# Performance work log

Measured on AMD Instinct MI355X. Metric: run time of the kernel, lower is better.

The kernel has to match this reference:

```python
import jax, jax.numpy as jnp
import numpy as np

B, L, HID = 2, 2048, 2048
N_HEAD, HEAD_DIM, N_KV = 32, 64, 8
N_Q_PER_KV = N_HEAD // N_KV  # 4
SCALE = 0.125  # 1/sqrt(HEAD_DIM)
PAD_START = L - 256  # last 256 key positions are padding
NEG = -1e9


def setup_inputs() -> dict:
    key = jax.random.key(0)
    ks = jax.random.split(key, 8)
    query = jax.random.normal(ks[0], (B, L, HID), jnp.float32)
    kv = jax.random.normal(ks[1], (B, L, HID), jnp.float32)
    # additive causal mask (0 on/below diagonal, -1e9 above)
    i = jnp.arange(L)
    attn_mask = jnp.where(i[None, :] > i[:, None], NEG, 0.0).astype(jnp.float32)
    # key padding mask: True == padded position
    key_padding_mask = (i[None, :] >= PAD_START) & jnp.ones((B, 1), bool)
    s = 0.02
    Wq = jax.random.normal(ks[2], (HID, N_HEAD * HEAD_DIM), jnp.float32) * s
    bq = jnp.zeros((N_HEAD * HEAD_DIM,), jnp.float32)
    Wkv = jax.random.normal(ks[3], (HID, 2 * N_KV * HEAD_DIM), jnp.float32) * s
    bkv = jnp.zeros((2 * N_KV * HEAD_DIM,), jnp.float32)
    Wo = jax.random.normal(ks[4], (N_HEAD * HEAD_DIM, HID), jnp.float32) * s
    bo = jnp.zeros((HID,), jnp.float32)
    return {"query": query, "kv": kv, "Wq": Wq, "bq": bq, "Wkv": Wkv,
            "bkv": bkv, "Wo": Wo, "bo": bo, "attn_mask": attn_mask,
            "key_padding_mask": key_padding_mask}


def reference(query, kv, Wq, bq, Wkv, bkv, Wo, bo, attn_mask, key_padding_mask):
    b, l, _ = query.shape
    q = (query @ Wq + bq).reshape(b, l, N_HEAD, HEAD_DIM).transpose(0, 2, 1, 3)  # [B,H,L,D]
    kvp = kv @ Wkv + bkv                                   # [B,L,2*NKV*D]
    k, v = jnp.split(kvp, 2, axis=-1)
    k = k.reshape(b, l, N_KV, HEAD_DIM)
    v = v.reshape(b, l, N_KV, HEAD_DIM)
    # GQA: repeat_interleave KV heads to match Q heads
    k = jnp.repeat(k, N_Q_PER_KV, axis=2).transpose(0, 2, 1, 3)  # [B,H,L,D]
    v = jnp.repeat(v, N_Q_PER_KV, axis=2).transpose(0, 2, 1, 3)
    qk = jnp.einsum('bhqd,bhkd->bhqk', q, k) * SCALE
    qk = qk + attn_mask                                     # additive mask
    qk = jnp.where(key_padding_mask[:, None, None, :], NEG, qk)
    p = jax.nn.softmax(qk.astype(jnp.float32), axis=-1).astype(q.dtype)
    attn = jnp.einsum('bhqk,bhkd->bhqd', p, v)
    attn = attn.transpose(0, 2, 1, 3).reshape(b, l, N_HEAD * HEAD_DIM)
    out = attn @ Wo + bo
    return out
```

## Files before the change

kernel.cpp:

```cpp
#include <hip/hip_runtime.h>
#include <stdint.h>

#define L_SEQ 2048
#define HID 2048
#define PADK 1792
#define QSCALE 0.18033688011112042f

typedef unsigned short us_t;
typedef __attribute__((ext_vector_type(8))) short bf16x8;
typedef __attribute__((ext_vector_type(4))) float f32x4;

__device__ __forceinline__ float bf2f(us_t u) {
    union { unsigned int i; float f; } c; c.i = ((unsigned int)u) << 16; return c.f;
}
__device__ __forceinline__ us_t f2bf(float f) {
    union { float f; unsigned int i; } c; c.f = f;
    unsigned int i = c.i;
    return (us_t)((i + 0x7FFFu + ((i >> 16) & 1u)) >> 16);
}
__device__ __forceinline__ unsigned int pk_bf16(float a, float b) {
#if __has_builtin(__builtin_amdgcn_cvt_pk_bf16_f32)
    auto r = __builtin_amdgcn_cvt_pk_bf16_f32(a, b);
    unsigned int u; __builtin_memcpy(&u, &r, 4); return u;
#else
    return (unsigned int)f2bf(a) | ((unsigned int)f2bf(b) << 16);
#endif
}
__device__ __forceinline__ float fast_exp2(float x) {
#if __has_builtin(__builtin_amdgcn_exp2f)
    return __builtin_amdgcn_exp2f(x);
#else
    return exp2f(x);
#endif
}
__device__ __forceinline__ void gload_lds16(const us_t* g, us_t* l) {
    __builtin_amdgcn_global_load_lds((const __attribute__((address_space(1))) void*)g,
                                     (__attribute__((address_space(3))) void*)l, 16, 0, 0);
}
__device__ __forceinline__ int detect_bf16(const unsigned int* q) {
    __shared__ int sc[4];
    unsigned int v = q[threadIdx.x & 255];
    unsigned int e = (v >> 7) & 0xFFu;
    unsigned long long bb = __ballot(e >= 112u && e <= 133u);
    int cnt = __popcll(bb);
    if ((threadIdx.x & 63) == 0) sc[threadIdx.x >> 6] = cnt;
    __syncthreads();
    return (sc[0] + sc[1] + sc[2] + sc[3]) > 128;
}

__global__ __launch_bounds__(256) void prep(const unsigned int* __restrict__ qdet,
                                            const void* __restrict__ query,
                                            const void* __restrict__ kvsrc,
                                            const void* __restrict__ Wq,
                                            const void* __restrict__ Wkv,
                                            const void* __restrict__ Wo,
                                            us_t* __restrict__ Aq, us_t* __restrict__ Akv,
                                            us_t* __restrict__ Wqt, us_t* __restrict__ Wkvt,
                                            us_t* __restrict__ Wot) {
    __shared__ us_t tile[64][65];
    const int bf = detect_bf16(qdet);
    int id = blockIdx.x;
    if (id < 8192) {
        const void* s = (id < 4096) ? query : kvsrc;
        us_t* d       = (id < 4096) ? Aq : Akv;
        int cid = (id & 4095) * 256 + threadIdx.x;
        if (bf) {
            ((bf16x8*)d)[cid] = ((const bf16x8*)s)[cid];
        } else {
            const float* sp = (const float*)s + (size_t)cid * 8;
            f32x4 a = *(const f32x4*)sp, b2 = *(const f32x4*)(sp + 4);
            union { bf16x8 v; unsigned int dw[4]; } o;
            o.dw[0] = pk_bf16(a[0], a[1]);   o.dw[1] = pk_bf16(a[2], a[3]);
            o.dw[2] = pk_bf16(b2[0], b2[1]); o.dw[3] = pk_bf16(b2[2], b2[3]);
            ((bf16x8*)d)[cid] = o.v;
        }
        return;
    }
    id -= 8192;
    const void* s; us_t* d; int R, C, bx, by;
    if (id < 1024)      { s = Wq;  d = Wqt;  R = 2048; C = 2048; bx = id & 31; by = id >> 5; }
    else if (id < 1536) { id -= 1024; s = Wkv; d = Wkvt; R = 2048; C = 1024; bx = id & 15; by = id >> 4; }
    else                { id -= 1536; s = Wo;  d = Wot;  R = 2048; C = 2048; bx = id & 31; by = id >> 5; }
    const int c0 = bx * 64, r0 = by * 64;
    #pragma unroll
    for (int i = 0; i < 16; ++i) {
        int idx = threadIdx.x + i * 256;
        int r = idx >> 6, c = idx & 63;
        tile[r][c] = bf ? ((const us_t*)s)[(size_t)(r0 + r) * C + c0 + c]
                        : f2bf(((const float*)s)[(size_t)(r0 + r) * C + c0 + c]);
    }
    __syncthreads();
    #pragma unroll
    for (int i = 0; i < 16; ++i) {
        int idx = threadIdx.x + i * 256;
        int c = idx >> 6, r = idx & 63;
        d[(size_t)(c0 + c) * R + r0 + r] = tile[r][c];
    }
}

__device__ __forceinline__ void gemm_core(const us_t* __restrict__ A,
                                          const us_t* __restrict__ Bt,
                                          int K, int bm, int bn, int t,
                                          us_t (&As)[2][8192], us_t (&Bs)[2][8192],
                                          f32x4 (&acc)[4][4]) {
    const int w = t >> 6, lane = t & 63, l15 = lane & 15, quad = lane >> 4;
    const int wm = (w & 1) * 64, wn = (w >> 1) * 64;
    int rA[4], cA[4];
    #pragma unroll
    for (int i = 0; i < 4; ++i) {
        int p = (w * 4 + i) * 64 + lane;
        int row = p >> 3, cs = p & 7;
        rA[i] = row; cA[i] = (cs ^ (row & 7)) * 8;
    }
    #pragma unroll
    for (int i = 0; i < 4; ++i) {
        gload_lds16(A  + (size_t)(bm + rA[i]) * K + cA[i], &As[0][(w * 4 + i) * 512]);
        gload_lds16(Bt + (size_t)(bn + rA[i]) * K + cA[i], &Bs[0][(w * 4 + i) * 512]);
    }
    int pb = 0;
    for (int k0 = 0; k0 < K; k0 += 64) {
        __syncthreads();
        if (k0 + 64 < K) {
            #pragma unroll
            for (int i = 0; i < 4; ++i) {
                gload_lds16(A  + (size_t)(bm + rA[i]) * K + k0 + 64 + cA[i], &As[pb ^ 1][(w * 4 + i) * 512]);
                gload_lds16(Bt + (size_t)(bn + rA[i]) * K + k0 + 64 + cA[i], &Bs[pb ^ 1][(w * 4 + i) * 512]);
            }
        }
        #pragma unroll
        for (int ki = 0; ki < 2; ++ki) {
            bf16x8 af[4], bfr[4];
            #pragma unroll
            for (int mt = 0; mt < 4; ++mt) {
                int row = wm + mt * 16 + l15;
                int cs  = (ki * 4 + quad) ^ (row & 7);
                af[mt] = *(const bf16x8*)&As[pb][row * 64 + cs * 8];
            }
            #pragma unroll
            for (int nt = 0; nt < 4; ++nt) {
                int row = wn + nt * 16 + l15;
                int cs  = (ki * 4 + quad) ^ (row & 7);
                bfr[nt] = *(const bf16x8*)&Bs[pb][row * 64 + cs * 8];
            }
            #pragma unroll
            for (int mt = 0; mt < 4; ++mt)
                #pragma unroll
                for (int nt = 0; nt < 4; ++nt)
                    acc[mt][nt] = __builtin_amdgcn_mfma_f32_16x16x32_bf16(af[mt], bfr[nt], acc[mt][nt], 0, 0, 0);
        }
        pb ^= 1;
    }
}

__global__ __launch_bounds__(256, 2) void qkv_gemm(const unsigned int* __restrict__ qdet,
                                                   const us_t* __restrict__ Aq,
                                                   const us_t* __restrict__ Akv,
                                                   const us_t* __restrict__ Wqt,
                                                   const us_t* __restrict__ Wkvt,
                                                   const void* __restrict__ bq,
                                                   const void* __restrict__ bkv,
                                                   us_t* __restrict__ Qm,
                                                   us_t* __restrict__ Km,
                                                   us_t* __restrict__ Vg) {
    __shared__ us_t As[2][8192], Bs[2][8192];
    const int bf = detect_bf16(qdet);
    const int t = threadIdx.x;
    const int w = t >> 6, lane = t & 63, l15 = lane & 15, quad = lane >> 4;
    const int wm = (w & 1) * 64, wn = (w >> 1) * 64;
    f32x4 acc[4][4];
    #pragma unroll
    for (int i = 0; i < 4; ++i)
        #pragma unroll
        for (int j = 0; j < 4; ++j) acc[i][j] = (f32x4){0.f, 0.f, 0.f, 0.f};

    int id = blockIdx.x;
    if (id < 512) {
        const int bm = (id >> 4) * 128, bn = (id & 15) * 128;
        gemm_core(Aq, Wqt, 2048, bm, bn, t, As, Bs, acc);
        #pragma unroll
        for (int nt = 0; nt < 4; ++nt) {
            int col = bn + wn + nt * 16 + l15;
            float bvv = bf ? bf2f(((const us_t*)bq)[col]) : ((const float*)bq)[col];
            #pragma unroll
            for (int mt = 0; mt < 4; ++mt)
                #pragma unroll
                for (int r = 0; r < 4; ++r) {
                    int row = bm + wm + mt * 16 + quad * 4 + r;
                    Qm[(size_t)row * 2048 + col] = f2bf((acc[mt][nt][r] + bvv) * QSCALE);
                }
        }
    } else {
        id -= 512;
        const int bm = (id >> 3) * 128, bn = (id & 7) * 128;
        gemm_core(Akv, Wkvt, 2048, bm, bn, t, As, Bs, acc);
        if (bn < 512) {
            #pragma unroll
            for (int nt = 0; nt < 4; ++nt) {
                int col = bn + wn + nt * 16 + l15;
                float bvv = bf ? bf2f(((const us_t*)bkv)[col]) : ((const float*)bkv)[col];
                #pragma unroll
                for (int mt = 0; mt < 4; ++mt)
                    #pragma unroll
                    for (int r = 0; r < 4; ++r) {
                        int row = bm + wm + mt * 16 + quad * 4 + r;
                        Km[(size_t)row * 512 + col] = f2bf(acc[mt][nt][r] + bvv);
                    }
            }
        } else {
            us_t* ldsT = &As[0][0];
            const int b2 = bm >> 11, tok0 = bm & 2047;
            #pragma unroll
            for (int hh = 0; hh < 2; ++hh) {
                __syncthreads();
                if ((w >> 1) == hh) {
                    #pragma unroll
                    for (int nt = 0; nt < 4; ++nt) {
                        int col = bn + hh * 64 + nt * 16 + l15;
                        float bvv = bf ? bf2f(((const us_t*)bkv)[col]) : ((const float*)bkv)[col];
                        int c2 = nt * 16 + l15;
                        #pragma unroll
                        for (int mt = 0; mt < 4; ++mt)
                            #pragma unroll
                            for (int r = 0; r < 4; ++r) {
                                int tok = wm + mt * 16 + quad * 4 + r;
                                ldsT[c2 * 136 + tok] = f2bf(acc[mt][nt][r] + bvv);
                            }
                    }
                }
                __syncthreads();
                size_t vrow0 = (size_t)(b2 * 512 + (bn - 512) + hh * 64);
                #pragma unroll
                for (int j = 0; j < 4; ++j) {
                    int idx = t + j * 256;
                    int c2 = idx >> 4, ch = idx & 15;
                    bf16x8 vv = *(const bf16x8*)&ldsT[c2 * 136 + ch * 8];
                    *(bf16x8*)(Vg + (vrow0 + c2) * (size_t)2048 + tok0 + ch * 8) = vv;
                }
            }
        }
    }
}

__global__ __launch_bounds__(256, 2) void o_gemm(const unsigned int* __restrict__ qdet,
                                                 const us_t* __restrict__ Ao,
                                                 const us_t* __restrict__ Wot,
                                                 const void* __restrict__ bo,
                                                 void* __restrict__ Out) {
    __shared__ us_t As[2][8192], Bs[2][8192];
    const int bf = detect_bf16(qdet);
    const int t = threadIdx.x;
    const int w = t >> 6, lane = t & 63, l15 = lane & 15, quad = lane >> 4;
    const int wm = (w & 1) * 64, wn = (w >> 1) * 64;
    const int bm = blockIdx.y * 128, bn = blockIdx.x * 128;
    f32x4 acc[4][4];
    #pragma unroll
    for (int i = 0; i < 4; ++i)
        #pragma unroll
        for (int j = 0; j < 4; ++j) acc[i][j] = (f32x4){0.f, 0.f, 0.f, 0.f};
    gemm_core(Ao, Wot, 2048, bm, bn, t, As, Bs, acc);
    #pragma unroll
    for (int nt = 0; nt < 4; ++nt) {
        int col = bn + wn + nt * 16 + l15;
        float bvv = bf ? bf2f(((const us_t*)bo)[col]) : ((const float*)bo)[col];
        #pragma unroll
        for (int mt = 0; mt < 4; ++mt)
            #pragma unroll
            for (int r = 0; r < 4; ++r) {
                int row = bm + wm + mt * 16 + quad * 4 + r;
                float v = acc[mt][nt][r] + bvv;
                if (bf) ((us_t*)Out)[(size_t)row * 2048 + col] = f2bf(v);
                else    ((float*)Out)[(size_t)row * 2048 + col] = v;
            }
    }
}

__device__ __forceinline__ void qk_exp(const bf16x8 kb[2][4], const bf16x8 qf[2][2],
                                       int q0, int k0, int l15, int quad,
                                       bf16x8 pa[2][2]) {
    f32x4 sa[2][4];
    #pragma unroll
    for (int mt = 0; mt < 2; ++mt)
        #pragma unroll
        for (int nt = 0; nt < 4; ++nt) sa[mt][nt] = (f32x4){0.f, 0.f, 0.f, 0.f};
    #pragma unroll
    for (int ki = 0; ki < 2; ++ki)
        #pragma unroll
        for (int mt = 0; mt < 2; ++mt)
            #pragma unroll
            for (int nt = 0; nt < 4; ++nt)
                sa[mt][nt] = __builtin_amdgcn_mfma_f32_16x16x32_bf16(kb[ki][nt], qf[mt][ki], sa[mt][nt], 0, 0, 0);
    const bool nm = (k0 + 63 > q0);
    #pragma unroll
    for (int mt = 0; mt < 2; ++mt) {
        const int qrow = q0 + mt * 16 + l15;
        union { bf16x8 v; unsigned int dw[4]; } u;
        #pragma unroll
        for (int k2 = 0; k2 < 2; ++k2) {
            #pragma unroll
            for (int hf = 0; hf < 2; ++hf) {
                const int nt = k2 * 2 + hf;
                const int keyb = k0 + k2 * 32 + hf * 4 + quad * 8;
                float e[4];
                #pragma unroll
                for (int r = 0; r < 4; ++r) {
                    float s = sa[mt][nt][r];
                    if (nm && (keyb + r > qrow)) s = -1e30f;
                    e[r] = fast_exp2(s);
                }
                u.dw[hf * 2]     = pk_bf16(e[0], e[1]);
                u.dw[hf * 2 + 1] = pk_bf16(e[2], e[3]);
            }
            pa[mt][k2] = u.v;
        }
    }
}

__global__ __launch_bounds__(256, 2) void attn_mfma(const us_t* __restrict__ Q,
                                                    const us_t* __restrict__ Km,
                                                    const us_t* __restrict__ Vg,
                                                    us_t* __restrict__ Am) {
    __shared__ us_t Ks[2][4096];
    __shared__ us_t Vt[2][4096];

    const int bid = blockIdx.x;
    const int pr  = bid & 31;
    const int kvh = (bid >> 5) & 7;
    const int b   = bid >> 8;
    const int t = threadIdx.x, w = t >> 6, lane = t & 63, l15 = lane & 15, quad = lane >> 4;
    const int h = kvh * 4 + w;
    const int q0h = 2016 - 32 * pr, q0l = 32 * pr;
    const int kend0 = min(q0h + 32, PADK), kend1 = min(q0l + 32, PADK);

    bf16x8 ones;
    #pragma unroll
    for (int j = 0; j < 8; ++j) ones[j] = (short)0x3F80;

    const us_t* Kbase = Km + (size_t)(b * L_SEQ) * 512 + kvh * 64;
    const us_t* Vbase = Vg + (size_t)(b * 512 + kvh * 64) * L_SEQ;

    size_t ksrc[2], vsrc[2];
    #pragma unroll
    for (int i = 0; i < 2; ++i) {
        int idx = (w * 2 + i) * 64 + lane;
        int p = idx >> 3, cs = idx & 7, c = cs ^ (p & 7);
        int gk = (p & 0x23) | ((p & 0x0C) << 1) | ((p & 0x10) >> 2);
        ksrc[i] = (size_t)gk * 512 + c * 8;
        vsrc[i] = (size_t)p * 2048 + c * 8;
    }

    bf16x8 qfh[2][2], qfl[2][2];
    #pragma unroll
    for (int mt = 0; mt < 2; ++mt)
        #pragma unroll
        for (int ki = 0; ki < 2; ++ki) {
            qfh[mt][ki] = *(const bf16x8*)(Q + (size_t)(b * L_SEQ + q0h + mt * 16 + l15) * HID
                                             + h * 64 + ki * 32 + quad * 8);
            qfl[mt][ki] = *(const bf16x8*)(Q + (size_t)(b * L_SEQ + q0l + mt * 16 + l15) * HID
                                             + h * 64 + ki * 32 + quad * 8);
        }

    f32x4 oah[2][4], oal[2][4], lah[2], lal[2];
    #pragma unroll
    for (int mt = 0; mt < 2; ++mt) {
        lah[mt] = (f32x4){0.f, 0.f, 0.f, 0.f};
        lal[mt] = (f32x4){0.f, 0.f, 0.f, 0.f};
        #pragma unroll
        for (int dn = 0; dn < 4; ++dn) {
            oah[mt][dn] = (f32x4){0.f, 0.f, 0.f, 0.f};
            oal[mt][dn] = (f32x4){0.f, 0.f, 0.f, 0.f};
        }
    }

    #pragma unroll
    for (int i = 0; i < 2; ++i) {
        gload_lds16(Kbase + ksrc[i], &Ks[0][(w * 2 + i) * 512]);
        gload_lds16(Vbase + vsrc[i], &Vt[0][(w * 2 + i) * 512]);
    }

    int pb = 0;
    for (int k0 = 0; k0 < kend0; k0 += 64) {
        __syncthreads();
        if (k0 + 64 < kend0) {
            #pragma unroll
            for (int i = 0; i < 2; ++i) {
                gload_lds16(Kbase + (size_t)(k0 + 64) * 512 + ksrc[i], &Ks[pb ^ 1][(w * 2 + i) * 512]);
                gload_lds16(Vbase + (k0 + 64) + vsrc[i],               &Vt[pb ^ 1][(w * 2 + i) * 512]);
            }
        }
        const bool dolight = (k0 < kend1);

        bf16x8 kb[2][4];
        #pragma unroll
        for (int ki = 0; ki < 2; ++ki)
            #pragma unroll
            for (int nt = 0; nt < 4; ++nt) {
                int row = nt * 16 + l15;
                int cs  = (ki * 4 + quad) ^ (row & 7);
                kb[ki][nt] = *(const bf16x8*)&Ks[pb][row * 64 + cs * 8];
            }

        bf16x8 pah[2][2], pal[2][2];
        qk_exp(kb, qfh, q0h, k0, l15, quad, pah);
        if (dolight) qk_exp(kb, qfl, q0l, k0, l15, quad, pal);

        bf16x8 vb[2][4];
        #pragma unroll
        for (int k2 = 0; k2 < 2; ++k2)
            #pragma unroll
            for (int dn = 0; dn < 4; ++dn) {
                int d  = dn * 16 + l15;
                int cs = (k2 * 4 + quad) ^ (d & 7);
                vb[k2][dn] = *(const bf16x8*)&Vt[pb][d * 64 + cs * 8];
            }

        #pragma unroll
        for (int k2 = 0; k2 < 2; ++k2)
            #pragma unroll
            for (int mt = 0; mt < 2; ++mt) {
                lah[mt] = __builtin_amdgcn_mfma_f32_16x16x32_bf16(pah[mt][k2], ones, lah[mt], 0, 0, 0);
                #pragma unroll
                for (int dn = 0; dn < 4; ++dn)
                    oah[mt][dn] = __builtin_amdgcn_mfma_f32_16x16x32_bf16(pah[mt][k2], vb[k2][dn], oah[mt][dn], 0, 0, 0);
            }
        if (dolight) {
            #pragma unroll
            for (int k2 = 0; k2 < 2; ++k2)
                #pragma unroll
                for (int mt = 0; mt < 2; ++mt) {
                    lal[mt] = __builtin_amdgcn_mfma_f32_16x16x32_bf16(pal[mt][k2], ones, lal[mt], 0, 0, 0);
                    #pragma unroll
                    for (int dn = 0; dn < 4; ++dn)
                        oal[mt][dn] = __builtin_amdgcn_mfma_f32_16x16x32_bf16(pal[mt][k2], vb[k2][dn], oal[mt][dn], 0, 0, 0);
                }
        }
        pb ^= 1;
    }

    #pragma unroll
    for (int mt = 0; mt < 2; ++mt)
        #pragma unroll
        for (int r = 0; r < 4; ++r) {
            float invh = 1.0f / lah[mt][r];
            float invl = 1.0f / lal[mt][r];
            int rowh = q0h + mt * 16 + quad * 4 + r;
            int rowl = q0l + mt * 16 + quad * 4 + r;
            #pragma unroll
            for (int dn = 0; dn < 4; ++dn) {
                Am[(size_t)(b * L_SEQ + rowh) * HID + h * 64 + dn * 16 + l15] =
                    f2bf(oah[mt][dn][r] * invh);
                Am[(size_t)(b * L_SEQ + rowl) * HID + h * 64 + dn * 16 + l15] =
                    f2bf(oal[mt][dn][r] * invl);
            }
        }
}

extern "C" void kernel_launch(void* const* d_in, const int* in_sizes, int n_in,
                              void* d_out, int out_size, void* d_ws, size_t ws_size,
                              hipStream_t stream) {
    const void* query = d_in[0];
    const void* kv    = d_in[1];
    const void* Wq    = d_in[2];
    const void* bq    = d_in[3];
    const void* Wkv   = d_in[4];
    const void* bkv   = d_in[5];
    const void* Wo    = d_in[6];
    const void* bo    = d_in[7];
    const unsigned int* qdet = (const unsigned int*)query;

    char* p = (char*)d_ws;
    us_t* Qm   = (us_t*)p;                p += (size_t)4096 * 2048 * 2;
    us_t* Km   = (us_t*)p;                p += (size_t)4096 * 512 * 2;
    us_t* Vg   = (us_t*)p;                p += (size_t)1024 * 2048 * 2;
    us_t* AqAm = (us_t*)p;                p += (size_t)4096 * 2048 * 2;
    us_t* Akv  = (us_t*)p;                p += (size_t)4096 * 2048 * 2;
    us_t* Wqt  = (us_t*)p;                p += (size_t)2048 * 2048 * 2;
    us_t* Wkvt = (us_t*)p;                p += (size_t)1024 * 2048 * 2;
    us_t* Wot  = (us_t*)p;

    dim3 blk(256);
    prep<<<dim3(10752), blk, 0, stream>>>(qdet, query, kv, Wq, Wkv, Wo,
                                          AqAm, Akv, Wqt, Wkvt, Wot);
    qkv_gemm<<<dim3(768), blk, 0, stream>>>(qdet, AqAm, Akv, Wqt, Wkvt, bq, bkv,
                                            Qm, Km, Vg);
    attn_mfma<<<dim3(512), blk, 0, stream>>>(Qm, Km, Vg, AqAm);
    o_gemm<<<dim3(16, 32), blk, 0, stream>>>(qdet, AqAm, Wot, bo, d_out);
}
```

Baseline: 361.0 us.

## Rewrite QKV GEMM as 256x256 tile, 8-wave kernel with phased prefetch

Replaces the 128x128, 4-wave QKV projection GEMM with a 256x256-tile, 512-thread kernel. The K loop is split into eight phases per pair of k-tiles, each interleaving partial global-to-LDS staging with MFMA bursts, using raw barriers, explicit vmcnt waits and setprio. The aim is more reuse per loaded tile and better overlap of loads with compute. The trade-off is 128KB of LDS, which may limit occupancy to one block per CU, and only 192 blocks on a 256-CU device.

```diff
diff --git a/kernel.cpp b/kernel.cpp
--- a/kernel.cpp
+++ b/kernel.cpp
@@ -46,6 +46,19 @@
     if ((threadIdx.x & 63) == 0) sc[threadIdx.x >> 6] = cnt;
     __syncthreads();
     return (sc[0] + sc[1] + sc[2] + sc[3]) > 128;
+}
+__device__ __forceinline__ int detect_bf16_512(const unsigned int* q) {
+    __shared__ int sc[8];
+    unsigned int v = q[threadIdx.x & 255];
+    unsigned int e = (v >> 7) & 0xFFu;
+    unsigned long long bb = __ballot(e >= 112u && e <= 133u);
+    int cnt = __popcll(bb);
+    if ((threadIdx.x & 63) == 0) sc[threadIdx.x >> 6] = cnt;
+    __syncthreads();
+    int s = 0;
+    #pragma unroll
+    for (int i = 0; i < 8; ++i) s += sc[i];
+    return s > 256;
 }
 
 __global__ __launch_bounds__(256) void prep(const unsigned int* __restrict__ qdet,
@@ -98,61 +111,42 @@
     }
 }
 
-__device__ __forceinline__ void gemm_core(const us_t* __restrict__ A,
-                                          const us_t* __restrict__ Bt,
-                                          int K, int bm, int bn, int t,
-                                          us_t (&As)[2][8192], us_t (&Bs)[2][8192],
-                                          f32x4 (&acc)[4][4]) {
-    const int w = t >> 6, lane = t & 63, l15 = lane & 15, quad = lane >> 4;
-    const int wm = (w & 1) * 64, wn = (w >> 1) * 64;
-    int rA[4], cA[4];
-    #pragma unroll
-    for (int i = 0; i < 4; ++i) {
-        int p = (w * 4 + i) * 64 + lane;
-        int row = p >> 3, cs = p & 7;
-        rA[i] = row; cA[i] = (cs ^ (row & 7)) * 8;
-    }
-    #pragma unroll
-    for (int i = 0; i < 4; ++i) {
-        gload_lds16(A  + (size_t)(bm + rA[i]) * K + cA[i], &As[0][(w * 4 + i) * 512]);
-        gload_lds16(Bt + (size_t)(bn + rA[i]) * K + cA[i], &Bs[0][(w * 4 + i) * 512]);
-    }
-    int pb = 0;
-    for (int k0 = 0; k0 < K; k0 += 64) {
-        __syncthreads();
-        if (k0 + 64 < K) {
-            #pragma unroll
-            for (int i = 0; i < 4; ++i) {
-                gload_lds16(A  + (size_t)(bm + rA[i]) * K + k0 + 64 + cA[i], &As[pb ^ 1][(w * 4 + i) * 512]);
-                gload_lds16(Bt + (size_t)(bn + rA[i]) * K + k0 + 64 + cA[i], &Bs[pb ^ 1][(w * 4 + i) * 512]);
-            }
-        }
-        #pragma unroll
-        for (int ki = 0; ki < 2; ++ki) {
-            bf16x8 af[4], bfr[4];
-            #pragma unroll
-            for (int mt = 0; mt < 4; ++mt) {
-                int row = wm + mt * 16 + l15;
-                int cs  = (ki * 4 + quad) ^ (row & 7);
-                af[mt] = *(const bf16x8*)&As[pb][row * 64 + cs * 8];
-            }
-            #pragma unroll
-            for (int nt = 0; nt < 4; ++nt) {
-                int row = wn + nt * 16 + l15;
-                int cs  = (ki * 4 + quad) ^ (row & 7);
-                bfr[nt] = *(const bf16x8*)&Bs[pb][row * 64 + cs * 8];
-            }
-            #pragma unroll
-            for (int mt = 0; mt < 4; ++mt)
-                #pragma unroll
-                for (int nt = 0; nt < 4; ++nt)
-                    acc[mt][nt] = __builtin_amdgcn_mfma_f32_16x16x32_bf16(af[mt], bfr[nt], acc[mt][nt], 0, 0, 0);
-        }
-        pb ^= 1;
-    }
-}
-
-__global__ __launch_bounds__(256, 2) void qkv_gemm(const unsigned int* __restrict__ qdet,
+template<int MQ, int NQ, typename STG, typename TAIL>
+__device__ __forceinline__ void phase8(const us_t* Ab, const us_t* Bb,
+                                       int wm, int wn, int l15, int cs0, int cs1,
+                                       f32x4 (&acc)[8][4], STG&& stg, TAIL&& tail) {
+    bf16x8 af[4][2], bv[2][2];
+    #pragma unroll
+    for (int mt = 0; mt < 4; ++mt) {
+        const us_t* p = &Ab[(wm * 128 + MQ * 64 + mt * 16 + l15) * 64];
+        af[mt][0] = *(const bf16x8*)&p[cs0 * 8];
+        af[mt][1] = *(const bf16x8*)&p[cs1 * 8];
+    }
+    #pragma unroll
+    for (int nt = 0; nt < 2; ++nt) {
+        const us_t* p = &Bb[(wn * 64 + NQ * 32 + nt * 16 + l15) * 64];
+        bv[nt][0] = *(const bf16x8*)&p[cs0 * 8];
+        bv[nt][1] = *(const bf16x8*)&p[cs1 * 8];
+    }
+    stg();
+    __builtin_amdgcn_s_barrier();
+    asm volatile("s_waitcnt lgkmcnt(0)" ::: "memory");
+    __builtin_amdgcn_sched_barrier(0);
+    __builtin_amdgcn_s_setprio(1);
+    #pragma unroll
+    for (int ki = 0; ki < 2; ++ki)
+        #pragma unroll
+        for (int mt = 0; mt < 4; ++mt)
+            #pragma unroll
+            for (int nt = 0; nt < 2; ++nt)
+                acc[MQ * 4 + mt][NQ * 2 + nt] = __builtin_amdgcn_mfma_f32_16x16x32_bf16(
+                    af[mt][ki], bv[nt][ki], acc[MQ * 4 + mt][NQ * 2 + nt], 0, 0, 0);
+    __builtin_amdgcn_s_setprio(0);
+    tail();
+    __builtin_amdgcn_s_barrier();
+}
+
+__global__ __launch_bounds__(512, 2) void qkv_gemm(const unsigned int* __restrict__ qdet,
                                                    const us_t* __restrict__ Aq,
                                                    const us_t* __restrict__ Akv,
                                                    const us_t* __restrict__ Wqt,
@@ -162,82 +156,199 @@
                                                    us_t* __restrict__ Qm,
                                                    us_t* __restrict__ Km,
                                                    us_t* __restrict__ Vg) {
-    __shared__ us_t As[2][8192], Bs[2][8192];
-    const int bf = detect_bf16(qdet);
+    __shared__ us_t sh[65536];
+    us_t* As0 = sh;
+    us_t* As1 = sh + 16384;
+    us_t* Bs0 = sh + 32768;
+    us_t* Bs1 = sh + 49152;
+
+    const int bf = detect_bf16_512(qdet);
     const int t = threadIdx.x;
     const int w = t >> 6, lane = t & 63, l15 = lane & 15, quad = lane >> 4;
+    const int wm = w >> 2, wn = w & 3;
+    const int cs0 = quad ^ (l15 & 7);
+    const int cs1 = (4 + quad) ^ (l15 & 7);
+
+    int id = blockIdx.x;
+    const us_t* Ag; const us_t* Bg; int bm, bn; bool isQ;
+    if (id < 128) { isQ = true;  Ag = Aq;  Bg = Wqt;  bm = (id >> 3) * 256; bn = (id & 7) * 256; }
+    else { id -= 128; isQ = false; Ag = Akv; Bg = Wkvt; bm = (id >> 2) * 256; bn = (id & 3) * 256; }
+
+    size_t aoff[2][2], boff[2][2]; int adst[2][2], bdst[2][2];
+    #pragma unroll
+    for (int u = 0; u < 2; ++u)
+        #pragma unroll
+        for (int j = 0; j < 2; ++j) {
+            int row0 = j * 128 + u * 64 + w * 8;
+            int row  = row0 + (lane >> 3);
+            int col  = ((lane & 7) ^ (row & 7)) * 8;
+            aoff[u][j] = (size_t)(bm + row) * 2048 + col;
+            adst[u][j] = row0 * 64;
+            int ci   = w * 2 + j;
+            int rb0  = (ci >> 2) * 64 + u * 32 + (ci & 3) * 8;
+            int rowb = rb0 + (lane >> 3);
+            int colb = ((lane & 7) ^ (rowb & 7)) * 8;
+            boff[u][j] = (size_t)(bn + rowb) * 2048 + colb;
+            bdst[u][j] = rb0 * 64;
+        }
+
+#define STAGE_A(U, KT, DST) do { \
+        gload_lds16(Ag + aoff[U][0] + (size_t)(KT) * 64, (DST) + adst[U][0]); \
+        gload_lds16(Ag + aoff[U][1] + (size_t)(KT) * 64, (DST) + adst[U][1]); } while (0)
+#define STAGE_B(U, KT, DST) do { \
+        gload_lds16(Bg + boff[U][0] + (size_t)(KT) * 64, (DST) + bdst[U][0]); \
+        gload_lds16(Bg + boff[U][1] + (size_t)(KT) * 64, (DST) + bdst[U][1]); } while (0)
+
+    f32x4 acc[8][4];
+    #pragma unroll
+    for (int i = 0; i < 8; ++i)
+        #pragma unroll
+        for (int j = 0; j < 4; ++j) acc[i][j] = (f32x4){0.f, 0.f, 0.f, 0.f};
+
+    STAGE_A(0, 0, As0); STAGE_B(0, 0, Bs0);
+    STAGE_A(1, 0, As0); STAGE_B(1, 0, Bs0);
+    STAGE_A(0, 1, As1); STAGE_B(0, 1, Bs1);
+    asm volatile("s_waitcnt vmcnt(4)" ::: "memory");
+    __builtin_amdgcn_s_barrier();
+
+    auto notail = [] {};
+    #pragma unroll 1
+    for (int it = 0; it < 16; ++it) {
+        const bool more = (it < 15);
+        const int k1 = 2 * it + 1, k2 = 2 * it + 2, k3 = 2 * it + 3;
+        phase8<0, 0>(As0, Bs0, wm, wn, l15, cs0, cs1, acc,
+                     [&] { STAGE_A(1, k1, As1); }, notail);
+        phase8<0, 1>(As0, Bs0, wm, wn, l15, cs0, cs1, acc,
+                     [&] { STAGE_B(1, k1, Bs1); }, notail);
+        phase8<1, 0>(As0, Bs0, wm, wn, l15, cs0, cs1, acc,
+                     [&] { if (more) STAGE_A(0, k2, As0); }, notail);
+        phase8<1, 1>(As0, Bs0, wm, wn, l15, cs0, cs1, acc,
+                     [&] { if (more) STAGE_B(0, k2, Bs0); },
+                     [&] { if (more) asm volatile("s_waitcnt vmcnt(4)" ::: "memory");
+                           else      asm volatile("s_waitcnt vmcnt(0)" ::: "memory"); });
+        phase8<0, 0>(As1, Bs1, wm, wn, l15, cs0, cs1, acc,
+                     [&] { if (more) STAGE_A(1, k2, As0); }, notail);
+        phase8<0, 1>(As1, Bs1, wm, wn, l15, cs0, cs1, acc,
+                     [&] { if (more) STAGE_B(1, k2, Bs0); }, notail);
+        phase8<1, 0>(As1, Bs1, wm, wn, l15, cs0, cs1, acc,
+                     [&] { if (more) STAGE_A(0, k3, As1); }, notail);
+        phase8<1, 1>(As1, Bs1, wm, wn, l15, cs0, cs1, acc,
+                     [&] { if (more) STAGE_B(0, k3, Bs1); },
+                     [&] { if (more) asm volatile("s_waitcnt vmcnt(4)" ::: "memory"); });
+    }
+#undef STAGE_A
+#undef STAGE_B
+
+    if (isQ) {
+        #pragma unroll
+        for (int an = 0; an < 4; ++an) {
+            int col = bn + wn * 64 + an * 16 + l15;
+            float bvv = bf ? bf2f(((const us_t*)bq)[col]) : ((const float*)bq)[col];
+            #pragma unroll
+            for (int am = 0; am < 8; ++am)
+                #pragma unroll
+                for (int r = 0; r < 4; ++r) {
+                    int row = bm + wm * 128 + am * 16 + quad * 4 + r;
+                    Qm[(size_t)row * 2048 + col] = f2bf((acc[am][an][r] + bvv) * QSCALE);
+                }
+        }
+    } else if (bn < 512) {
+        #pragma unroll
+        for (int an = 0; an < 4; ++an) {
+            int col = bn + wn * 64 + an * 16 + l15;
+            float bvv = bf ? bf2f(((const us_t*)bkv)[col]) : ((const float*)bkv)[col];
+            #pragma unroll
+            for (int am = 0; am < 8; ++am)
+                #pragma unroll
+                for (int r = 0; r < 4; ++r) {
+                    int row = bm + wm * 128 + am * 16 + quad * 4 + r;
+                    Km[(size_t)row * 512 + col] = f2bf(acc[am][an][r] + bvv);
+                }
+        }
+    } else {
+        const int b2 = bm >> 11, tok0 = bm & 2047;
+        #pragma unroll
+        for (int half = 0; half < 2; ++half) {
+            __syncthreads();
+            if ((wn >> 1) == half) {
+                #pragma unroll
+                for (int an = 0; an < 4; ++an) {
+                    int col = bn + wn * 64 + an * 16 + l15;
+                    float bvv = bf ? bf2f(((const us_t*)bkv)[col]) : ((const float*)bkv)[col];
+                    int cl = (wn & 1) * 64 + an * 16 + l15;
+                    #pragma unroll
+                    for (int am = 0; am < 8; ++am)
+                        #pragma unroll
+                        for (int r = 0; r < 4; ++r) {
+                            int tok = wm * 128 + am * 16 + quad * 4 + r;
+                            sh[cl * 258 + tok] = f2bf(acc[am][an][r] + bvv);
+                        }
+                }
+            }
+            __syncthreads();
+            size_t vrow0 = (size_t)(b2 * 512 + (bn - 512) + half * 128);
+            #pragma unroll
+            for (int jj = 0; jj < 8; ++jj) {
+                int idx = t + jj * 512;
+                int c2 = idx >> 5, ch = idx & 31;
+                bf16x8 vv = *(const bf16x8*)&sh[c2 * 258 + ch * 8];
+                *(bf16x8*)(Vg + (vrow0 + c2) * (size_t)2048 + tok0 + ch * 8) = vv;
+            }
+        }
+    }
+}
+
+__device__ __forceinline__ void gemm_core(const us_t* __restrict__ A,
+                                          const us_t* __restrict__ Bt,
+                                          int K, int bm, int bn, int t,
+                                          us_t (&As)[2][8192], us_t (&Bs)[2][8192],
+                                          f32x4 (&acc)[4][4]) {
+    const int w = t >> 6, lane = t & 63, l15 = lane & 15, quad = lane >> 4;
     const int wm = (w & 1) * 64, wn = (w >> 1) * 64;
-    f32x4 acc[4][4];
-    #pragma unroll
-    for (int i = 0; i < 4; ++i)
-        #pragma unroll
-        for (int j = 0; j < 4; ++j) acc[i][j] = (f32x4){0.f, 0.f, 0.f, 0.f};
-
-    int id = blockIdx.x;
-    if (id < 512) {
-        const int bm = (id >> 4) * 128, bn = (id & 15) * 128;
-        gemm_core(Aq, Wqt, 2048, bm, bn, t, As, Bs, acc);
-        #pragma unroll
-        for (int nt = 0; nt < 4; ++nt) {
-            int col = bn + wn + nt * 16 + l15;
-            float bvv = bf ? bf2f(((const us_t*)bq)[col]) : ((const float*)bq)[col];
+    int rA[4], cA[4];
+    #pragma unroll
+    for (int i = 0; i < 4; ++i) {
+        int p = (w * 4 + i) * 64 + lane;
+        int row = p >> 3, cs = p & 7;
+        rA[i] = row; cA[i] = (cs ^ (row & 7)) * 8;
+    }
+    #pragma unroll
+    for (int i = 0; i < 4; ++i) {
+        gload_lds16(A  + (size_t)(bm + rA[i]) * K + cA[i], &As[0][(w * 4 + i) * 512]);
+        gload_lds16(Bt + (size_t)(bn + rA[i]) * K + cA[i], &Bs[0][(w * 4 + i) * 512]);
+    }
+    int pb = 0;
+    for (int k0 = 0; k0 < K; k0 += 64) {
+        __syncthreads();
+        if (k0 + 64 < K) {
+            #pragma unroll
+            for (int i = 0; i < 4; ++i) {
+                gload_lds16(A  + (size_t)(bm + rA[i]) * K + k0 + 64 + cA[i], &As[pb ^ 1][(w * 4 + i) * 512]);
+                gload_lds16(Bt + (size_t)(bn + rA[i]) * K + k0 + 64 + cA[i], &Bs[pb ^ 1][(w * 4 + i) * 512]);
+            }
+        }
+        #pragma unroll
+        for (int ki = 0; ki < 2; ++ki) {
+            bf16x8 af[4], bfr[4];
+            #pragma unroll
+            for (int mt = 0; mt < 4; ++mt) {
+                int row = wm + mt * 16 + l15;
+                int cs  = (ki * 4 + quad) ^ (row & 7);
+                af[mt] = *(const bf16x8*)&As[pb][row * 64 + cs * 8];
+            }
+            #pragma unroll
+            for (int nt = 0; nt < 4; ++nt) {
+                int row = wn + nt * 16 + l15;
+                int cs  = (ki * 4 + quad) ^ (row & 7);
+                bfr[nt] = *(const bf16x8*)&Bs[pb][row * 64 + cs * 8];
+            }
             #pragma unroll
             for (int mt = 0; mt < 4; ++mt)
                 #pragma unroll
-                for (int r = 0; r < 4; ++r) {
-                    int row = bm + wm + mt * 16 + quad * 4 + r;
-                    Qm[(size_t)row * 2048 + col] = f2bf((acc[mt][nt][r] + bvv) * QSCALE);
-                }
-        }
-    } else {
-        id -= 512;
-        const int bm = (id >> 3) * 128, bn = (id & 7) * 128;
-        gemm_core(Akv, Wkvt, 2048, bm, bn, t, As, Bs, acc);
-        if (bn < 512) {
-            #pragma unroll
-            for (int nt = 0; nt < 4; ++nt) {
-                int col = bn + wn + nt * 16 + l15;
-                float bvv = bf ? bf2f(((const us_t*)bkv)[col]) : ((const float*)bkv)[col];
-                #pragma unroll
-                for (int mt = 0; mt < 4; ++mt)
-                    #pragma unroll
-                    for (int r = 0; r < 4; ++r) {
-                        int row = bm + wm + mt * 16 + quad * 4 + r;
-                        Km[(size_t)row * 512 + col] = f2bf(acc[mt][nt][r] + bvv);
-                    }
-            }
-        } else {
-            us_t* ldsT = &As[0][0];
-            const int b2 = bm >> 11, tok0 = bm & 2047;
-            #pragma unroll
-            for (int hh = 0; hh < 2; ++hh) {
-                __syncthreads();
-                if ((w >> 1) == hh) {
-                    #pragma unroll
-                    for (int nt = 0; nt < 4; ++nt) {
-                        int col = bn + hh * 64 + nt * 16 + l15;
-                        float bvv = bf ? bf2f(((const us_t*)bkv)[col]) : ((const float*)bkv)[col];
-                        int c2 = nt * 16 + l15;
-                        #pragma unroll
-                        for (int mt = 0; mt < 4; ++mt)
-                            #pragma unroll
-                            for (int r = 0; r < 4; ++r) {
-                                int tok = wm + mt * 16 + quad * 4 + r;
-                                ldsT[c2 * 136 + tok] = f2bf(acc[mt][nt][r] + bvv);
-                            }
-                    }
-                }
-                __syncthreads();
-                size_t vrow0 = (size_t)(b2 * 512 + (bn - 512) + hh * 64);
-                #pragma unroll
-                for (int j = 0; j < 4; ++j) {
-                    int idx = t + j * 256;
-                    int c2 = idx >> 4, ch = idx & 15;
-                    bf16x8 vv = *(const bf16x8*)&ldsT[c2 * 136 + ch * 8];
-                    *(bf16x8*)(Vg + (vrow0 + c2) * (size_t)2048 + tok0 + ch * 8) = vv;
-                }
-            }
-        }
+                for (int nt = 0; nt < 4; ++nt)
+                    acc[mt][nt] = __builtin_amdgcn_mfma_f32_16x16x32_bf16(af[mt], bfr[nt], acc[mt][nt], 0, 0, 0);
+        }
+        pb ^= 1;
     }
 }
 
@@ -480,8 +591,8 @@
     dim3 blk(256);
     prep<<<dim3(10752), blk, 0, stream>>>(qdet, query, kv, Wq, Wkv, Wo,
                                           AqAm, Akv, Wqt, Wkvt, Wot);
-    qkv_gemm<<<dim3(768), blk, 0, stream>>>(qdet, AqAm, Akv, Wqt, Wkvt, bq, bkv,
-                                            Qm, Km, Vg);
+    qkv_gemm<<<dim3(192), dim3(512), 0, stream>>>(qdet, AqAm, Akv, Wqt, Wkvt, bq, bkv,
+                                                  Qm, Km, Vg);
     attn_mfma<<<dim3(512), blk, 0, stream>>>(Qm, Km, Vg, AqAm);
     o_gemm<<<dim3(16, 32), blk, 0, stream>>>(qdet, AqAm, Wot, bo, d_out);
 }
```

After: 363.9 us. Within noise of the previous version (+0.8%).
